# Kernel tuning notes

Measured on AMD Instinct MI355X. Metric: run time of the kernel, lower is better.

The kernel has to match this reference:

```python
import jax, jax.numpy as jnp
import numpy as np

B, N, K, D = 16, 8192, 20, 64  # batch, points, neighbors, feature dim
LN_EPS = 1e-5


def setup_inputs() -> dict:
    key = jax.random.key(0)
    k1, k2, k3 = jax.random.split(key, 3)
    x = jax.random.normal(k1, (B, N, D), dtype=jnp.float32)
    neighbor_ind = jax.random.randint(k2, (B, N, K), 0, N)
    # torch Linear(2D -> D, bias=False): weight shape (out=D, in=2D), y = feat @ W.T
    W = jax.random.normal(k3, (D, 2 * D), dtype=jnp.float32) * (1.0 / np.sqrt(2 * D))
    gamma = jnp.ones((D,), jnp.float32)
    beta = jnp.zeros((D,), jnp.float32)
    return {"x": x, "neighbor_ind": neighbor_ind, "W": W, "gamma": gamma, "beta": beta}


def reference(x, neighbor_ind, W, gamma, beta):
    # route(): gather neighbor features and build [neighbor - center, center]
    neighbor_x = jax.vmap(lambda xb, ib: xb[ib])(x, neighbor_ind)        # (b, n, k, d)
    center = x[:, :, None, :]                                            # (b, n, 1, d)
    feat = jnp.concatenate(
        [neighbor_x - center, jnp.broadcast_to(center, neighbor_x.shape)], axis=-1
    )                                                                    # (b, n, k, 2d)
    # per-edge Linear (bias=False), then max over k neighbors
    h = jnp.einsum('bnke,oe->bnko', feat, W)                             # (b, n, k, d)
    h = h.max(axis=2)                                                    # (b, n, d)
    # LayerNorm over last dim, then exact GELU
    mu = h.mean(axis=-1, keepdims=True)
    var = jnp.mean((h - mu) ** 2, axis=-1, keepdims=True)
    hn = (h - mu) * jax.lax.rsqrt(var + LN_EPS) * gamma + beta
    return jax.nn.gelu(hn, approximate=False)
```

## Files before the change

kernel.cpp:

```cpp
#include <hip/hip_runtime.h>
#include <math.h>

#define B_ 16
#define N_ 8192
#define K_ 20
#define NPTS (B_ * N_)

typedef __attribute__((ext_vector_type(4))) float f4;
typedef __attribute__((ext_vector_type(8))) short s8;
typedef __attribute__((ext_vector_type(4))) unsigned int u4;
typedef __attribute__((ext_vector_type(4))) unsigned short us4;

__device__ __forceinline__ unsigned short f2bf(float f) {
    union { float f; unsigned u; } v; v.f = f;
    return (unsigned short)((v.u + 0x7FFFu + ((v.u >> 16) & 1u)) >> 16);
}
__device__ __forceinline__ float bfhi(unsigned w) { return __uint_as_float(w & 0xFFFF0000u); }
__device__ __forceinline__ float bflo(unsigned w) { return __uint_as_float(w << 16); }

__global__ __launch_bounds__(256) void prep_kernel(const float* __restrict__ W,
                                                   unsigned short* __restrict__ Wg) {
    const int i = blockIdx.x * 256 + threadIdx.x;
    const int j = i >> 6, d = i & 63;
    const float v = (j < 64) ? W[j * 128 + d]
                             : (W[(j - 64) * 128 + 64 + d] - W[(j - 64) * 128 + d]);
    Wg[i] = f2bf(v);
}

__global__ __launch_bounds__(256) void proj_kernel(const float* __restrict__ x,
                                                   const unsigned short* __restrict__ Wg,
                                                   unsigned short* __restrict__ Y1,
                                                   unsigned short* __restrict__ Bs) {
    __shared__ unsigned short Wl[128 * 72];
    const int t = threadIdx.x;

    for (int i = t; i < 1024; i += 256) {
        u4 v = ((const u4*)Wg)[i];
        *((u4*)((char*)Wl + (i >> 3) * 144 + (i & 7) * 16)) = v;
    }
    __syncthreads();

    const int lane = t & 63;
    const int wv = t >> 6;
    const int m = lane & 15;
    const int q = lane >> 4;
    const int pbase = blockIdx.x * 64 + wv * 16;

    const float* xr = x + (size_t)(pbase + m) * 64 + q * 8;
    f4 x0 = *(const f4*)(xr);
    f4 x1 = *(const f4*)(xr + 4);
    f4 x2 = *(const f4*)(xr + 32);
    f4 x3 = *(const f4*)(xr + 36);
    s8 X0, X1;
    X0[0]=(short)f2bf(x0.x); X0[1]=(short)f2bf(x0.y); X0[2]=(short)f2bf(x0.z); X0[3]=(short)f2bf(x0.w);
    X0[4]=(short)f2bf(x1.x); X0[5]=(short)f2bf(x1.y); X0[6]=(short)f2bf(x1.z); X0[7]=(short)f2bf(x1.w);
    X1[0]=(short)f2bf(x2.x); X1[1]=(short)f2bf(x2.y); X1[2]=(short)f2bf(x2.z); X1[3]=(short)f2bf(x2.w);
    X1[4]=(short)f2bf(x3.x); X1[5]=(short)f2bf(x3.y); X1[6]=(short)f2bf(x3.z); X1[7]=(short)f2bf(x3.w);

    f4 acc[8];
#pragma unroll
    for (int tt = 0; tt < 8; ++tt) acc[tt] = (f4)0.f;

#pragma unroll
    for (int s = 0; s < 2; ++s) {
        const s8 X = s ? X1 : X0;
#pragma unroll
        for (int tt = 0; tt < 8; ++tt) {
            s8 w = *(const s8*)((const char*)Wl + (16 * tt + m) * 144 + s * 64 + q * 16);
            acc[tt] = __builtin_amdgcn_mfma_f32_16x16x32_bf16(w, X, acc[tt], 0, 0, 0);
        }
    }

    const size_t prow = (size_t)(pbase + m) * 64;
#pragma unroll
    for (int tt = 0; tt < 4; ++tt) {
        us4 u;
        u.x = f2bf(acc[tt][0]); u.y = f2bf(acc[tt][1]);
        u.z = f2bf(acc[tt][2]); u.w = f2bf(acc[tt][3]);
        *(us4*)&Y1[prow + tt * 16 + q * 4] = u;
    }
#pragma unroll
    for (int tt = 4; tt < 8; ++tt) {
        us4 u;
        u.x = f2bf(acc[tt][0]); u.y = f2bf(acc[tt][1]);
        u.z = f2bf(acc[tt][2]); u.w = f2bf(acc[tt][3]);
        *(us4*)&Bs[prow + (tt - 4) * 16 + q * 4] = u;
    }
}

__global__ __launch_bounds__(256) void gather_kernel(const unsigned short* __restrict__ Y1,
                                                     const unsigned short* __restrict__ Bs,
                                                     const int* __restrict__ ind,
                                                     const float* __restrict__ gamma,
                                                     const float* __restrict__ beta,
                                                     float* __restrict__ out) {
    const int lane = threadIdx.x & 63;
    const int wave = threadIdx.x >> 6;
    const int sub = lane & 7;
    const int q = lane >> 3;
    const int bi = blockIdx.x;
    const int bt = bi & 15;
    const int jj = bi >> 4;
    const int p = bt * N_ + jj * 32 + wave * 8 + q;
    const int bbase = bt * N_ * 64;

    int idxs[K_];
    const int4* ip = (const int4*)&ind[p * K_];
#pragma unroll
    for (int v = 0; v < 5; ++v) {
        int4 iv = ip[v];
        idxs[4 * v + 0] = iv.x; idxs[4 * v + 1] = iv.y;
        idxs[4 * v + 2] = iv.z; idxs[4 * v + 3] = iv.w;
    }

    f4 ma = (f4)(-INFINITY), mb = (f4)(-INFINITY);
#pragma unroll
    for (int r = 0; r < 2; ++r) {
        u4 rv[10];
#pragma unroll
        for (int k = 0; k < 10; ++k)
            rv[k] = *(const u4*)(Y1 + bbase + idxs[r * 10 + k] * 64 + sub * 8);
#pragma unroll
        for (int k = 0; k < 10; ++k) {
            ma.x = fmaxf(ma.x, bflo(rv[k].x)); ma.y = fmaxf(ma.y, bfhi(rv[k].x));
            ma.z = fmaxf(ma.z, bflo(rv[k].y)); ma.w = fmaxf(ma.w, bfhi(rv[k].y));
            mb.x = fmaxf(mb.x, bflo(rv[k].z)); mb.y = fmaxf(mb.y, bfhi(rv[k].z));
            mb.z = fmaxf(mb.z, bflo(rv[k].w)); mb.w = fmaxf(mb.w, bfhi(rv[k].w));
        }
    }

    u4 bsv = __builtin_nontemporal_load((const u4*)(Bs + (size_t)p * 64 + sub * 8));
    f4 ha, hb;
    ha.x = ma.x + bflo(bsv.x); ha.y = ma.y + bfhi(bsv.x);
    ha.z = ma.z + bflo(bsv.y); ha.w = ma.w + bfhi(bsv.y);
    hb.x = mb.x + bflo(bsv.z); hb.y = mb.y + bfhi(bsv.z);
    hb.z = mb.z + bflo(bsv.w); hb.w = mb.w + bfhi(bsv.w);

    float s = ha.x + ha.y + ha.z + ha.w + hb.x + hb.y + hb.z + hb.w;
#pragma unroll
    for (int off = 4; off >= 1; off >>= 1) s += __shfl_xor(s, off, 64);
    const float mu = s * (1.0f / 64.0f);
    f4 da = ha - mu, db = hb - mu;
    float v2 = da.x * da.x + da.y * da.y + da.z * da.z + da.w * da.w
             + db.x * db.x + db.y * db.y + db.z * db.z + db.w * db.w;
#pragma unroll
    for (int off = 4; off >= 1; off >>= 1) v2 += __shfl_xor(v2, off, 64);
    const float rstd = rsqrtf(v2 * (1.0f / 64.0f) + 1e-5f);

    const f4 g0 = *(const f4*)&gamma[sub * 8];
    const f4 g1 = *(const f4*)&gamma[sub * 8 + 4];
    const f4 b0 = *(const f4*)&beta[sub * 8];
    const f4 b1 = *(const f4*)&beta[sub * 8 + 4];
    f4 na = da * rstd * g0 + b0;
    f4 nb = db * rstd * g1 + b1;

    f4 r0, r1;
    r0.x = 0.5f * na.x * (1.0f + erff(na.x * 0.70710678f));
    r0.y = 0.5f * na.y * (1.0f + erff(na.y * 0.70710678f));
    r0.z = 0.5f * na.z * (1.0f + erff(na.z * 0.70710678f));
    r0.w = 0.5f * na.w * (1.0f + erff(na.w * 0.70710678f));
    r1.x = 0.5f * nb.x * (1.0f + erff(nb.x * 0.70710678f));
    r1.y = 0.5f * nb.y * (1.0f + erff(nb.y * 0.70710678f));
    r1.z = 0.5f * nb.z * (1.0f + erff(nb.z * 0.70710678f));
    r1.w = 0.5f * nb.w * (1.0f + erff(nb.w * 0.70710678f));
    float* op = &out[(size_t)p * 64 + sub * 8];
    __builtin_nontemporal_store(r0, (f4*)op);
    __builtin_nontemporal_store(r1, (f4*)(op + 4));
}

extern "C" void kernel_launch(void* const* d_in, const int* in_sizes, int n_in,
                              void* d_out, int out_size, void* d_ws, size_t ws_size,
                              hipStream_t stream) {
    const float* x     = (const float*)d_in[0];
    const int*   ind   = (const int*)d_in[1];
    const float* W     = (const float*)d_in[2];
    const float* gamma = (const float*)d_in[3];
    const float* beta  = (const float*)d_in[4];
    float* out = (float*)d_out;

    unsigned short* Bs = (unsigned short*)d_ws;
    unsigned short* Y1 = Bs + (size_t)NPTS * 64;
    unsigned short* Wg = Y1 + (size_t)NPTS * 64;

    prep_kernel<<<32, 256, 0, stream>>>(W, Wg);
    proj_kernel<<<NPTS / 64, 256, 0, stream>>>(x, Wg, Y1, Bs);
    gather_kernel<<<NPTS / 32, 256, 0, stream>>>(Y1, Bs, ind, gamma, beta, out);
}
```

Baseline: 125.6 us.

## Fold weight prep into projection kernel, use max3 and nontemporal loads

Removes the separate prep kernel: each projection block now reads fp32 W directly, forms the combined weight (W_center - W_neighbor for the second half), converts it to bf16 and writes it into shared memory. This drops one kernel launch and one small workspace round trip, at the cost of every block redoing the weight transform and reading twice as many bytes of W. The gather kernel's max reduction now uses an inline v_max3_f32 so each instruction folds two neighbors. Loads of x and of the neighbor indices become nontemporal to limit cache pollution from streamed data.

New measurement: 137.8 us. +9.7%, slower.

```diff
diff --git a/kernel.cpp b/kernel.cpp
--- a/kernel.cpp
+++ b/kernel.cpp
@@ -10,6 +10,7 @@
 typedef __attribute__((ext_vector_type(8))) short s8;
 typedef __attribute__((ext_vector_type(4))) unsigned int u4;
 typedef __attribute__((ext_vector_type(4))) unsigned short us4;
+typedef __attribute__((ext_vector_type(4))) int i4;
 
 __device__ __forceinline__ unsigned short f2bf(float f) {
     union { float f; unsigned u; } v; v.f = f;
@@ -17,26 +18,32 @@
 }
 __device__ __forceinline__ float bfhi(unsigned w) { return __uint_as_float(w & 0xFFFF0000u); }
 __device__ __forceinline__ float bflo(unsigned w) { return __uint_as_float(w << 16); }
-
-__global__ __launch_bounds__(256) void prep_kernel(const float* __restrict__ W,
-                                                   unsigned short* __restrict__ Wg) {
-    const int i = blockIdx.x * 256 + threadIdx.x;
-    const int j = i >> 6, d = i & 63;
-    const float v = (j < 64) ? W[j * 128 + d]
-                             : (W[(j - 64) * 128 + 64 + d] - W[(j - 64) * 128 + d]);
-    Wg[i] = f2bf(v);
+__device__ __forceinline__ float max3f(float a, float b, float c) {
+    float d;
+    asm("v_max3_f32 %0, %1, %2, %3" : "=v"(d) : "v"(a), "v"(b), "v"(c));
+    return d;
 }
 
 __global__ __launch_bounds__(256) void proj_kernel(const float* __restrict__ x,
-                                                   const unsigned short* __restrict__ Wg,
+                                                   const float* __restrict__ W,
                                                    unsigned short* __restrict__ Y1,
                                                    unsigned short* __restrict__ Bs) {
     __shared__ unsigned short Wl[128 * 72];
     const int t = threadIdx.x;
 
-    for (int i = t; i < 1024; i += 256) {
-        u4 v = ((const u4*)Wg)[i];
-        *((u4*)((char*)Wl + (i >> 3) * 144 + (i & 7) * 16)) = v;
+    for (int i = t; i < 2048; i += 256) {
+        const int j = i >> 4, d0 = (i & 15) * 4;
+        f4 v;
+        if (j < 64) {
+            v = *(const f4*)&W[j * 128 + d0];
+        } else {
+            f4 a = *(const f4*)&W[(j - 64) * 128 + 64 + d0];
+            f4 c = *(const f4*)&W[(j - 64) * 128 + d0];
+            v = a - c;
+        }
+        us4 u;
+        u.x = f2bf(v.x); u.y = f2bf(v.y); u.z = f2bf(v.z); u.w = f2bf(v.w);
+        *(us4*)((char*)Wl + j * 144 + d0 * 2) = u;
     }
     __syncthreads();
 
@@ -47,10 +54,10 @@
     const int pbase = blockIdx.x * 64 + wv * 16;
 
     const float* xr = x + (size_t)(pbase + m) * 64 + q * 8;
-    f4 x0 = *(const f4*)(xr);
-    f4 x1 = *(const f4*)(xr + 4);
-    f4 x2 = *(const f4*)(xr + 32);
-    f4 x3 = *(const f4*)(xr + 36);
+    f4 x0 = __builtin_nontemporal_load((const f4*)(xr));
+    f4 x1 = __builtin_nontemporal_load((const f4*)(xr + 4));
+    f4 x2 = __builtin_nontemporal_load((const f4*)(xr + 32));
+    f4 x3 = __builtin_nontemporal_load((const f4*)(xr + 36));
     s8 X0, X1;
     X0[0]=(short)f2bf(x0.x); X0[1]=(short)f2bf(x0.y); X0[2]=(short)f2bf(x0.z); X0[3]=(short)f2bf(x0.w);
     X0[4]=(short)f2bf(x1.x); X0[5]=(short)f2bf(x1.y); X0[6]=(short)f2bf(x1.z); X0[7]=(short)f2bf(x1.w);
@@ -105,10 +112,10 @@
     const int bbase = bt * N_ * 64;
 
     int idxs[K_];
-    const int4* ip = (const int4*)&ind[p * K_];
+    const i4* ip = (const i4*)&ind[p * K_];
 #pragma unroll
     for (int v = 0; v < 5; ++v) {
-        int4 iv = ip[v];
+        i4 iv = __builtin_nontemporal_load(ip + v);
         idxs[4 * v + 0] = iv.x; idxs[4 * v + 1] = iv.y;
         idxs[4 * v + 2] = iv.z; idxs[4 * v + 3] = iv.w;
     }
@@ -121,11 +128,16 @@
         for (int k = 0; k < 10; ++k)
             rv[k] = *(const u4*)(Y1 + bbase + idxs[r * 10 + k] * 64 + sub * 8);
 #pragma unroll
-        for (int k = 0; k < 10; ++k) {
-            ma.x = fmaxf(ma.x, bflo(rv[k].x)); ma.y = fmaxf(ma.y, bfhi(rv[k].x));
-            ma.z = fmaxf(ma.z, bflo(rv[k].y)); ma.w = fmaxf(ma.w, bfhi(rv[k].y));
-            mb.x = fmaxf(mb.x, bflo(rv[k].z)); mb.y = fmaxf(mb.y, bfhi(rv[k].z));
-            mb.z = fmaxf(mb.z, bflo(rv[k].w)); mb.w = fmaxf(mb.w, bfhi(rv[k].w));
+        for (int k = 0; k < 10; k += 2) {
+            u4 a = rv[k], c = rv[k + 1];
+            ma.x = max3f(ma.x, bflo(a.x), bflo(c.x));
+            ma.y = max3f(ma.y, bfhi(a.x), bfhi(c.x));
+            ma.z = max3f(ma.z, bflo(a.y), bflo(c.y));
+            ma.w = max3f(ma.w, bfhi(a.y), bfhi(c.y));
+            mb.x = max3f(mb.x, bflo(a.z), bflo(c.z));
+            mb.y = max3f(mb.y, bfhi(a.z), bfhi(c.z));
+            mb.z = max3f(mb.z, bflo(a.w), bflo(c.w));
+            mb.w = max3f(mb.w, bfhi(a.w), bfhi(c.w));
         }
     }
 
@@ -180,9 +192,7 @@
 
     unsigned short* Bs = (unsigned short*)d_ws;
     unsigned short* Y1 = Bs + (size_t)NPTS * 64;
-    unsigned short* Wg = Y1 + (size_t)NPTS * 64;
 
-    prep_kernel<<<32, 256, 0, stream>>>(W, Wg);
-    proj_kernel<<<NPTS / 64, 256, 0, stream>>>(x, Wg, Y1, Bs);
+    proj_kernel<<<NPTS / 64, 256, 0, stream>>>(x, W, Y1, Bs);
     gather_kernel<<<NPTS / 32, 256, 0, stream>>>(Y1, Bs, ind, gamma, beta, out);
 }
```
